# Kernel optimization log

Hardware: AMD Instinct MI355X
Metric: run time of the kernel (lower is better)

Reference implementation:

```python
import jax, jax.numpy as jnp
import numpy as np

K = 512  # number of largest entries to KEEP per row (module's k)


def _topk_keep(x, k):
    """Zero all but the k largest entries along the last axis.

    Matches torch: topk(-x, dim-k) finds the (dim-k) smallest values of x
    and scatters 0 into them, keeping the k largest. We implement the
    equivalent keep-mask via top_k indices of x itself (ties resolved by
    index order, same as torch.topk).
    """
    shp = x.shape
    d = shp[-1]
    x2 = x.reshape(-1, d)                      # [N, d]
    _, idx = jax.lax.top_k(x2, k)              # [N, k] indices of largest
    rows = jnp.arange(x2.shape[0])[:, None]    # [N, 1]
    mask = jnp.zeros_like(x2).at[rows, idx].set(1.0)
    return (x2 * mask).reshape(shp)


def setup_inputs() -> dict:
    key = jax.random.key(0)
    x = jax.random.normal(key, (4, 4096, 4096), dtype=jnp.float32)
    return {"x": x}


def reference(x):
    return _topk_keep(x, K)
```

## Files before the change

kernel.cpp:

```cpp
#include <hip/hip_runtime.h>

#define D     4096
#define KKEEP 512
#define TPB   512
#define NSEG  2
#define NB    2048
#define BPT   (NB / TPB)
#define SALT  4
#define HWORDS (NB * SALT)
#define NWAVE (TPB / 64)

__device__ __forceinline__ unsigned key_of(float f) {
    unsigned u = __float_as_uint(f);
    return (u & 0x80000000u) ? ~u : (u | 0x80000000u);
}
__device__ __forceinline__ float val_of(unsigned k) {
    unsigned u = (k & 0x80000000u) ? (k ^ 0x80000000u) : ~k;
    return __uint_as_float(u);
}

__global__ __launch_bounds__(TPB, 4)
void topk_keep_kernel(const float* __restrict__ x, float* __restrict__ out) {
    const int tid = threadIdx.x;
    const unsigned lane = tid & 63u, wid = (unsigned)tid >> 6;
    const unsigned salt = lane & (SALT - 1u);
    const float4* px = (const float4*)(x + (long)blockIdx.x * D);
    float4*       po = (float4*)(out + (long)blockIdx.x * D);

    unsigned k[NSEG * 4];
    {
        float4 f0 = px[tid], f1 = px[tid + TPB];
        k[0]=key_of(f0.x); k[1]=key_of(f0.y); k[2]=key_of(f0.z); k[3]=key_of(f0.w);
        k[4]=key_of(f1.x); k[5]=key_of(f1.y); k[6]=key_of(f1.z); k[7]=key_of(f1.w);
    }

    __shared__ __align__(16) unsigned hist[HWORDS];
    __shared__ unsigned s_wtot[NWAVE];
    __shared__ unsigned s_sel[2];
    __shared__ unsigned s_p[NWAVE];

    unsigned prefix = 0;
    unsigned rem = KKEEP;

    #pragma unroll
    for (int r = 0; r < 3; ++r) {
        const int shift = (r == 0) ? 21 : (r == 1) ? 10 : 0;
        const unsigned mask = (r == 2) ? 1023u : 2047u;

        {
            uint4 z = make_uint4(0u, 0u, 0u, 0u);
            uint4* hz = (uint4*)&hist[tid * (BPT * SALT)];
            hz[0] = z; hz[1] = z; hz[2] = z; hz[3] = z;
        }
        __syncthreads();

        if (r == 0) {
            #pragma unroll
            for (int j = 0; j < 8; ++j) {
                unsigned b = k[j] >> 21;
                atomicAdd(&hist[(b << 2) | salt], 1u);
            }
        } else {
            const int hs = (r == 1) ? 21 : 10;
            #pragma unroll
            for (int j = 0; j < 8; ++j)
                if ((k[j] >> hs) == (prefix >> hs)) {
                    unsigned b = (k[j] >> shift) & mask;
                    atomicAdd(&hist[(b << 2) | salt], 1u);
                }
        }
        __syncthreads();

        unsigned c[BPT];
        unsigned ct = 0;
        {
            const uint4* hb = (const uint4*)&hist[tid * (BPT * SALT)];
            #pragma unroll
            for (int i = 0; i < BPT; ++i) {
                uint4 w = hb[i];
                c[i] = w.x + w.y + w.z + w.w;
                ct += c[i];
            }
        }
        unsigned s = ct;
        #pragma unroll
        for (int off = 1; off < 64; off <<= 1) {
            unsigned t = __shfl_down(s, off, 64);
            if (lane + (unsigned)off < 64u) s += t;
        }
        if (lane == 0) s_wtot[wid] = s;
        __syncthreads();
        unsigned above = s - ct;
        #pragma unroll
        for (unsigned w = 0; w < NWAVE; ++w)
            if (w > wid) above += s_wtot[w];
        unsigned run = above;
        #pragma unroll
        for (int i = BPT - 1; i >= 0; --i) {
            unsigned incl = run + c[i];
            if (incl >= rem && run < rem) {
                s_sel[0] = (unsigned)(tid * BPT + i);
                s_sel[1] = rem - run;
            }
            run = incl;
        }
        __syncthreads();
        prefix |= s_sel[0] << shift;
        rem = s_sel[1];
    }

    const unsigned tkey = prefix;

    unsigned e0 = (k[0]==tkey) + (k[1]==tkey) + (k[2]==tkey) + (k[3]==tkey);
    unsigned e1 = (k[4]==tkey) + (k[5]==tkey) + (k[6]==tkey) + (k[7]==tkey);
    unsigned p = e0 | (e1 << 16);
    unsigned ip = p;
    #pragma unroll
    for (int off = 1; off < 64; off <<= 1) {
        unsigned t = __shfl_up(ip, off, 64);
        if (lane >= (unsigned)off) ip += t;
    }
    if (lane == 63) s_p[wid] = ip;
    __syncthreads();
    unsigned xp = ip - p;
    #pragma unroll
    for (unsigned w = 0; w < NWAVE; ++w)
        if (w < wid) xp += s_p[w];
    unsigned tot = 0;
    #pragma unroll
    for (unsigned w = 0; w < NWAVE; ++w) tot += s_p[w];
    const unsigned total0 = tot & 0xffffu;
    unsigned rank[NSEG];
    rank[0] = xp & 0xffffu;
    rank[1] = total0 + (xp >> 16);

    #pragma unroll
    for (int j = 0; j < NSEG; ++j) {
        float4 o;
        unsigned eqr = rank[j];
        float* ofp = (float*)&o;
        #pragma unroll
        for (int c2 = 0; c2 < 4; ++c2) {
            unsigned kk = k[4*j + c2];
            bool keep;
            if (kk > tkey)       keep = true;
            else if (kk == tkey) { keep = (eqr < rem); ++eqr; }
            else                 keep = false;
            ofp[c2] = keep ? val_of(kk) : 0.0f;
        }
        po[tid + j * TPB] = o;
    }
}

extern "C" void kernel_launch(void* const* d_in, const int* in_sizes, int n_in,
                              void* d_out, int out_size, void* d_ws, size_t ws_size,
                              hipStream_t stream) {
    const float* x = (const float*)d_in[0];
    float* out = (float*)d_out;
    const int rows = in_sizes[0] / D;
    topk_keep_kernel<<<dim3(rows), dim3(TPB), 0, stream>>>(x, out);
}
```

Measured before the change: 534.0 us.

## Process two rows per block with packed dual-histogram radix select

```diff
diff --git a/kernel.cpp b/kernel.cpp
--- a/kernel.cpp
+++ b/kernel.cpp
@@ -3,11 +3,10 @@
 #define D     4096
 #define KKEEP 512
 #define TPB   512
-#define NSEG  2
 #define NB    2048
 #define BPT   (NB / TPB)
-#define SALT  4
-#define HWORDS (NB * SALT)
+#define HA(d) ((d) + ((d) >> 2))
+#define HWORDS (NB + NB / 4)
 #define NWAVE (TPB / 64)
 
 __device__ __forceinline__ unsigned key_of(float f) {
@@ -19,67 +18,78 @@
     return __uint_as_float(u);
 }
 
-__global__ __launch_bounds__(TPB, 4)
+__global__ __launch_bounds__(TPB, 8)
 void topk_keep_kernel(const float* __restrict__ x, float* __restrict__ out) {
     const int tid = threadIdx.x;
     const unsigned lane = tid & 63u, wid = (unsigned)tid >> 6;
-    const unsigned salt = lane & (SALT - 1u);
-    const float4* px = (const float4*)(x + (long)blockIdx.x * D);
-    float4*       po = (float4*)(out + (long)blockIdx.x * D);
-
-    unsigned k[NSEG * 4];
+    const long rowA = (long)blockIdx.x * 2;
+    const float4* pxA = (const float4*)(x + rowA * D);
+    const float4* pxB = pxA + (D / 4);
+    float4* poA = (float4*)(out + rowA * D);
+    float4* poB = poA + (D / 4);
+
+    unsigned ka[8], kb[8];
     {
-        float4 f0 = px[tid], f1 = px[tid + TPB];
-        k[0]=key_of(f0.x); k[1]=key_of(f0.y); k[2]=key_of(f0.z); k[3]=key_of(f0.w);
-        k[4]=key_of(f1.x); k[5]=key_of(f1.y); k[6]=key_of(f1.z); k[7]=key_of(f1.w);
-    }
-
-    __shared__ __align__(16) unsigned hist[HWORDS];
+        float4 a0 = pxA[tid], a1 = pxA[tid + TPB];
+        float4 b0 = pxB[tid], b1 = pxB[tid + TPB];
+        ka[0]=key_of(a0.x); ka[1]=key_of(a0.y); ka[2]=key_of(a0.z); ka[3]=key_of(a0.w);
+        ka[4]=key_of(a1.x); ka[5]=key_of(a1.y); ka[6]=key_of(a1.z); ka[7]=key_of(a1.w);
+        kb[0]=key_of(b0.x); kb[1]=key_of(b0.y); kb[2]=key_of(b0.z); kb[3]=key_of(b0.w);
+        kb[4]=key_of(b1.x); kb[5]=key_of(b1.y); kb[6]=key_of(b1.z); kb[7]=key_of(b1.w);
+    }
+
+    __shared__ unsigned hA[HWORDS], hB[HWORDS];
     __shared__ unsigned s_wtot[NWAVE];
-    __shared__ unsigned s_sel[2];
-    __shared__ unsigned s_p[NWAVE];
-
-    unsigned prefix = 0;
-    unsigned rem = KKEEP;
+    __shared__ unsigned s_sel[4];
+    __shared__ unsigned s_tA[NWAVE];
+    __shared__ unsigned s_tB[NWAVE];
+
+    #pragma unroll
+    for (int i = 0; i < HWORDS / TPB; ++i) {
+        hA[tid + i * TPB] = 0;
+        hB[tid + i * TPB] = 0;
+    }
+    __syncthreads();
+
+    unsigned prefA = 0, prefB = 0;
+    unsigned remA = KKEEP, remB = KKEEP;
 
     #pragma unroll
     for (int r = 0; r < 3; ++r) {
         const int shift = (r == 0) ? 21 : (r == 1) ? 10 : 0;
         const unsigned mask = (r == 2) ? 1023u : 2047u;
 
-        {
-            uint4 z = make_uint4(0u, 0u, 0u, 0u);
-            uint4* hz = (uint4*)&hist[tid * (BPT * SALT)];
-            hz[0] = z; hz[1] = z; hz[2] = z; hz[3] = z;
-        }
-        __syncthreads();
-
         if (r == 0) {
             #pragma unroll
             for (int j = 0; j < 8; ++j) {
-                unsigned b = k[j] >> 21;
-                atomicAdd(&hist[(b << 2) | salt], 1u);
+                atomicAdd(&hA[HA(ka[j] >> 21)], 1u);
+                atomicAdd(&hB[HA(kb[j] >> 21)], 1u);
             }
         } else {
             const int hs = (r == 1) ? 21 : 10;
             #pragma unroll
-            for (int j = 0; j < 8; ++j)
-                if ((k[j] >> hs) == (prefix >> hs)) {
-                    unsigned b = (k[j] >> shift) & mask;
-                    atomicAdd(&hist[(b << 2) | salt], 1u);
-                }
+            for (int j = 0; j < 8; ++j) {
+                if ((ka[j] >> hs) == (prefA >> hs))
+                    atomicAdd(&hA[HA((ka[j] >> shift) & mask)], 1u);
+                if ((kb[j] >> hs) == (prefB >> hs))
+                    atomicAdd(&hB[HA((kb[j] >> shift) & mask)], 1u);
+            }
         }
         __syncthreads();
 
         unsigned c[BPT];
         unsigned ct = 0;
         {
-            const uint4* hb = (const uint4*)&hist[tid * (BPT * SALT)];
+            const int hb = tid * 5;
             #pragma unroll
             for (int i = 0; i < BPT; ++i) {
-                uint4 w = hb[i];
-                c[i] = w.x + w.y + w.z + w.w;
+                unsigned cA = hA[hb + i], cB = hB[hb + i];
+                c[i] = cA | (cB << 16);
                 ct += c[i];
+            }
+            if (r < 2) {
+                #pragma unroll
+                for (int i = 0; i < BPT; ++i) { hA[hb + i] = 0; hB[hb + i] = 0; }
             }
         }
         unsigned s = ct;
@@ -94,61 +104,89 @@
         #pragma unroll
         for (unsigned w = 0; w < NWAVE; ++w)
             if (w > wid) above += s_wtot[w];
-        unsigned run = above;
+        unsigned runA = above & 0xffffu, runB = above >> 16;
         #pragma unroll
         for (int i = BPT - 1; i >= 0; --i) {
-            unsigned incl = run + c[i];
-            if (incl >= rem && run < rem) {
+            unsigned cA = c[i] & 0xffffu, cB = c[i] >> 16;
+            unsigned inclA = runA + cA;
+            if (inclA >= remA && runA < remA) {
                 s_sel[0] = (unsigned)(tid * BPT + i);
-                s_sel[1] = rem - run;
-            }
-            run = incl;
+                s_sel[1] = remA - runA;
+            }
+            runA = inclA;
+            unsigned inclB = runB + cB;
+            if (inclB >= remB && runB < remB) {
+                s_sel[2] = (unsigned)(tid * BPT + i);
+                s_sel[3] = remB - runB;
+            }
+            runB = inclB;
         }
         __syncthreads();
-        prefix |= s_sel[0] << shift;
-        rem = s_sel[1];
-    }
-
-    const unsigned tkey = prefix;
-
-    unsigned e0 = (k[0]==tkey) + (k[1]==tkey) + (k[2]==tkey) + (k[3]==tkey);
-    unsigned e1 = (k[4]==tkey) + (k[5]==tkey) + (k[6]==tkey) + (k[7]==tkey);
-    unsigned p = e0 | (e1 << 16);
-    unsigned ip = p;
+        prefA |= s_sel[0] << shift; remA = s_sel[1];
+        prefB |= s_sel[2] << shift; remB = s_sel[3];
+    }
+
+    const unsigned tkA = prefA, tkB = prefB;
+
+    unsigned eA0 = 0, eA1 = 0, eB0 = 0, eB1 = 0;
+    #pragma unroll
+    for (int c2 = 0; c2 < 4; ++c2) {
+        eA0 += (ka[c2] == tkA); eA1 += (ka[4 + c2] == tkA);
+        eB0 += (kb[c2] == tkB); eB1 += (kb[4 + c2] == tkB);
+    }
+    unsigned pA = eA0 | (eA1 << 16), pB = eB0 | (eB1 << 16);
+    unsigned iA = pA, iB = pB;
     #pragma unroll
     for (int off = 1; off < 64; off <<= 1) {
-        unsigned t = __shfl_up(ip, off, 64);
-        if (lane >= (unsigned)off) ip += t;
-    }
-    if (lane == 63) s_p[wid] = ip;
+        unsigned t0 = __shfl_up(iA, off, 64);
+        unsigned t1 = __shfl_up(iB, off, 64);
+        if (lane >= (unsigned)off) { iA += t0; iB += t1; }
+    }
+    if (lane == 63) { s_tA[wid] = iA; s_tB[wid] = iB; }
     __syncthreads();
-    unsigned xp = ip - p;
-    #pragma unroll
-    for (unsigned w = 0; w < NWAVE; ++w)
-        if (w < wid) xp += s_p[w];
-    unsigned tot = 0;
-    #pragma unroll
-    for (unsigned w = 0; w < NWAVE; ++w) tot += s_p[w];
-    const unsigned total0 = tot & 0xffffu;
-    unsigned rank[NSEG];
-    rank[0] = xp & 0xffffu;
-    rank[1] = total0 + (xp >> 16);
-
-    #pragma unroll
-    for (int j = 0; j < NSEG; ++j) {
+    unsigned xA = iA - pA, xB = iB - pB;
+    unsigned totA = 0, totB = 0;
+    #pragma unroll
+    for (unsigned w = 0; w < NWAVE; ++w) {
+        unsigned a = s_tA[w], b = s_tB[w];
+        if (w < wid) { xA += a; xB += b; }
+        totA += a; totB += b;
+    }
+    unsigned rankA[2], rankB[2];
+    rankA[0] = xA & 0xffffu; rankA[1] = (totA & 0xffffu) + (xA >> 16);
+    rankB[0] = xB & 0xffffu; rankB[1] = (totB & 0xffffu) + (xB >> 16);
+
+    #pragma unroll
+    for (int j = 0; j < 2; ++j) {
         float4 o;
-        unsigned eqr = rank[j];
+        unsigned eqr = rankA[j];
         float* ofp = (float*)&o;
         #pragma unroll
         for (int c2 = 0; c2 < 4; ++c2) {
-            unsigned kk = k[4*j + c2];
+            unsigned kk = ka[4 * j + c2];
             bool keep;
-            if (kk > tkey)       keep = true;
-            else if (kk == tkey) { keep = (eqr < rem); ++eqr; }
-            else                 keep = false;
+            if (kk > tkA)       keep = true;
+            else if (kk == tkA) { keep = (eqr < remA); ++eqr; }
+            else                keep = false;
             ofp[c2] = keep ? val_of(kk) : 0.0f;
         }
-        po[tid + j * TPB] = o;
+        poA[tid + j * TPB] = o;
+    }
+    #pragma unroll
+    for (int j = 0; j < 2; ++j) {
+        float4 o;
+        unsigned eqr = rankB[j];
+        float* ofp = (float*)&o;
+        #pragma unroll
+        for (int c2 = 0; c2 < 4; ++c2) {
+            unsigned kk = kb[4 * j + c2];
+            bool keep;
+            if (kk > tkB)       keep = true;
+            else if (kk == tkB) { keep = (eqr < remB); ++eqr; }
+            else                keep = false;
+            ofp[c2] = keep ? val_of(kk) : 0.0f;
+        }
+        poB[tid + j * TPB] = o;
     }
 }
 
@@ -158,5 +196,5 @@
     const float* x = (const float*)d_in[0];
     float* out = (float*)d_out;
     const int rows = in_sizes[0] / D;
-    topk_keep_kernel<<<dim3(rows), dim3(TPB), 0, stream>>>(x, out);
-}
+    topk_keep_kernel<<<dim3(rows / 2), dim3(TPB), 0, stream>>>(x, out);
+}
```

New measurement: 439.7 us. 17.7% less time.
